# Optimization experiments

Measured on AMD Instinct MI355X. Metric: run time of the kernel, lower is better.

Reference implementation:

```python
import jax, jax.numpy as jnp
import numpy as np
import math

N_HEAD = 16
N_KV = 4


def setup_inputs() -> dict:
    key = jax.random.key(0)
    ks = jax.random.split(key, 10)
    B, T, C = 4, 2048, 1024
    hd = C // N_HEAD
    kv_dim = N_KV * hd  # 256
    s = 0.02
    return {
        "x": jax.random.normal(ks[0], (B, T, C), jnp.float32),
        "Wq": jax.random.normal(ks[1], (C, C), jnp.float32) * s,
        "bq": jax.random.normal(ks[2], (C,), jnp.float32) * s,
        "Wk": jax.random.normal(ks[3], (kv_dim, C), jnp.float32) * s,
        "bk": jax.random.normal(ks[4], (kv_dim,), jnp.float32) * s,
        "Wv": jax.random.normal(ks[5], (kv_dim, C), jnp.float32) * s,
        "bv": jax.random.normal(ks[6], (kv_dim,), jnp.float32) * s,
        "Wo": jax.random.normal(ks[7], (C, C), jnp.float32) * s,
        "bo": jax.random.normal(ks[8], (C,), jnp.float32) * s,
        "qk_gain": jnp.full((N_HEAD,), 5.5, jnp.float32),
    }


def reference(x, Wq, bq, Wk, bk, Wv, bv, Wo, bo, qk_gain):
    B, T, C = x.shape
    H, KV = N_HEAD, N_KV
    hd = C // H
    G = H // KV  # GQA group size

    # Projections (torch Linear: y = x @ W.T + b)
    q = (x @ Wq.T + bq).reshape(B, T, KV, G, hd).transpose(0, 2, 3, 1, 4)  # [B,KV,G,T,hd]
    k = (x @ Wk.T + bk).reshape(B, T, KV, hd).transpose(0, 2, 1, 3)        # [B,KV,T,hd]
    v = (x @ Wv.T + bv).reshape(B, T, KV, hd).transpose(0, 2, 1, 3)        # [B,KV,T,hd]

    # per-head gain on q; head order h = kv*G + g matches repeat_interleave
    q = q * qk_gain.reshape(1, KV, G, 1, 1)

    # GQA: contract each query group against its shared kv head (no KV replication)
    att = jnp.einsum('bkgtd,bksd->bkgts', q, k) / math.sqrt(hd)  # [B,KV,G,T,T]
    causal = jnp.tril(jnp.ones((T, T), bool))
    att = jnp.where(causal, att, -jnp.inf)
    att = jax.nn.softmax(att, axis=-1)

    y = jnp.einsum('bkgts,bksd->bkgtd', att, v)          # [B,KV,G,T,hd]
    y = y.transpose(0, 3, 1, 2, 4).reshape(B, T, C)      # [B,T,C]
    return y @ Wo.T + bo
```

## Files before the change

kernel.cpp:

```cpp
#include <hip/hip_runtime.h>
#include <hip/hip_bf16.h>

typedef __attribute__((ext_vector_type(8))) short bf16x8;
typedef __attribute__((ext_vector_type(4))) float f32x4;
typedef __attribute__((ext_vector_type(16))) float f32x16;
typedef __attribute__((ext_vector_type(2))) unsigned uint2v;

#define DEVI static __device__ __forceinline__

constexpr int Bb = 4, Tt = 2048, Cc = 1024, Hh = 16;
constexpr int Mrows = Bb * Tt;
constexpr int KVdim = 256;
constexpr float LOG2E = 1.44269504088896340736f;

DEVI unsigned short f2bf(float f) {
  union { float f; unsigned u; } v; v.f = f;
  unsigned r = v.u + 0x7fffu + ((v.u >> 16) & 1u);
  return (unsigned short)(r >> 16);
}

DEVI f32x4 mfma16(bf16x8 a, bf16x8 b, f32x4 c) {
  return __builtin_amdgcn_mfma_f32_16x16x32_bf16(a, b, c, 0, 0, 0);
}
DEVI f32x16 mfma32(bf16x8 a, bf16x8 b, f32x16 c) {
  return __builtin_amdgcn_mfma_f32_32x32x16_bf16(a, b, c, 0, 0, 0);
}

DEVI unsigned cvtpk(float lo, float hi) {
  unsigned w;
  asm("v_cvt_pk_bf16_f32 %0, %1, %2" : "=v"(w) : "v"(lo), "v"(hi));
  return w;
}

DEVI void load_lds16(const void* g, void* s) {
  __builtin_amdgcn_global_load_lds(
      (const __attribute__((address_space(1))) void*)g,
      (__attribute__((address_space(3))) void*)s, 16, 0, 0);
}

__global__ __launch_bounds__(256) void cvt_all(
    const float* __restrict__ s0, const float* __restrict__ s1,
    const float* __restrict__ s2, const float* __restrict__ s3,
    const float* __restrict__ s4,
    unsigned short* __restrict__ d0, unsigned short* __restrict__ d1,
    unsigned short* __restrict__ d2, unsigned short* __restrict__ d3,
    unsigned short* __restrict__ d4,
    int n0, int n1, int n2, int n3, int n4) {
  const float* s; unsigned short* d; int n;
  switch (blockIdx.y) {
    case 0: s = s0; d = d0; n = n0; break;
    case 1: s = s1; d = d1; n = n1; break;
    case 2: s = s2; d = d2; n = n2; break;
    case 3: s = s3; d = d3; n = n3; break;
    default: s = s4; d = d4; n = n4; break;
  }
  int i = (blockIdx.x * 256 + threadIdx.x) * 4;
  const int stride = gridDim.x * 256 * 4;
  for (; i < n; i += stride) {
    float4 v = *(const float4*)(s + i);
    ushort4 o;
    o.x = f2bf(v.x); o.y = f2bf(v.y); o.z = f2bf(v.z); o.w = f2bf(v.w);
    *(ushort4*)(d + i) = o;
  }
}

__global__ __launch_bounds__(256, 4) void qkv_gemm(const short* __restrict__ A,
                                                const short* __restrict__ wq,
                                                const short* __restrict__ wk,
                                                const short* __restrict__ wv,
                                                const float* __restrict__ bq,
                                                const float* __restrict__ bk,
                                                const float* __restrict__ bv,
                                                const float* __restrict__ gain,
                                                unsigned short* __restrict__ qout,
                                                unsigned short* __restrict__ kout,
                                                unsigned short* __restrict__ vout) {
  constexpr int K = Cc;
  __shared__ __align__(16) union QkvSmem {
    struct { short As[128 * 64]; short Bs[128 * 64]; } g;
    unsigned short Ls[64][136];
  } sm;
  short* As = sm.g.As;
  short* Bs = sm.g.Bs;
  const int tid = threadIdx.x;
  const int w = tid >> 6, l = tid & 63;
  const int l15 = l & 15, lg = l >> 4;
  const int m0 = blockIdx.x * 128, n0 = blockIdx.y * 128;

  const short* Bsrc; const float* bias; int mode;
  if (n0 < 1024)      { Bsrc = wq + (size_t)n0 * K;          bias = bq + n0;          mode = 0; }
  else if (n0 < 1280) { Bsrc = wk + (size_t)(n0 - 1024) * K; bias = bk + (n0 - 1024); mode = 1; }
  else                { Bsrc = wv + (size_t)(n0 - 1280) * K; bias = bv + (n0 - 1280); mode = 2; }

  const int wr = (w >> 1) * 64, wc = (w & 1) * 64;
  f32x4 acc[4][4] = {};

  const int lrow = l >> 3;
  const int lchk = (l & 7) ^ (lrow & 7);
  const short* gA = A + (size_t)(m0 + w * 32 + lrow) * K + lchk * 8;
  const short* gB = Bsrc + (size_t)(w * 32 + lrow) * K + lchk * 8;
  short* lA = As + w * 32 * 64;
  short* lB = Bs + w * 32 * 64;
  const int sw = l15 & 7;

  for (int k0 = 0; k0 < K; k0 += 64) {
#pragma unroll
    for (int i = 0; i < 4; ++i) {
      load_lds16(gA + (size_t)i * 8 * K, lA + i * 8 * 64);
      load_lds16(gB + (size_t)i * 8 * K, lB + i * 8 * 64);
    }
    gA += 64; gB += 64;
    __syncthreads();
    bf16x8 af[2][4], bfr[2][4];
#pragma unroll
    for (int kk = 0; kk < 2; ++kk)
#pragma unroll
      for (int i = 0; i < 4; ++i) {
        const int ch = ((kk * 4 + lg) ^ sw) << 3;
        af[kk][i] = *(const bf16x8*)(As + (wr + i * 16 + l15) * 64 + ch);
        bfr[kk][i] = *(const bf16x8*)(Bs + (wc + i * 16 + l15) * 64 + ch);
      }
#pragma unroll
    for (int kk = 0; kk < 2; ++kk)
#pragma unroll
      for (int mi = 0; mi < 4; ++mi)
#pragma unroll
        for (int ni = 0; ni < 4; ++ni)
          acc[mi][ni] = mfma16(af[kk][mi], bfr[kk][ni], acc[mi][ni]);
    __syncthreads();
  }

  const int crow = m0 + wr + lg * 4;
  if (mode == 2) {
    const int bb2 = m0 >> 11, tt0 = m0 & (Tt - 1);
#pragma unroll
    for (int colHalf = 0; colHalf < 2; ++colHalf) {
      if (colHalf) __syncthreads();
      if ((w & 1) == colHalf) {
#pragma unroll
        for (int ni = 0; ni < 4; ++ni) {
          const int c = ni * 16 + l15;
          const float bv_ = bias[colHalf * 64 + c];
#pragma unroll
          for (int mi = 0; mi < 4; ++mi)
#pragma unroll
            for (int r = 0; r < 4; ++r)
              sm.Ls[c][wr + lg * 4 + mi * 16 + r] = f2bf(acc[mi][ni][r] + bv_);
        }
      }
      __syncthreads();
      const int c = tid >> 2, ch = tid & 3;
      const int vcol = (n0 - 1280) + colHalf * 64 + c;
      unsigned short* dst = vout +
          ((size_t)((bb2 * 4 + (vcol >> 6)) * 64 + (vcol & 63))) * Tt + tt0 + ch * 32;
      const unsigned short* src = &sm.Ls[c][ch * 32];
#pragma unroll
      for (int q = 0; q < 4; ++q)
        *(bf16x8*)(dst + q * 8) = *(const bf16x8*)(src + q * 8);
    }
    return;
  }
#pragma unroll
  for (int ni = 0; ni < 4; ++ni) {
    const int lcol = wc + ni * 16 + l15;
    const float bv_ = bias[lcol];
    float sc = 1.f;
    if (mode == 0) sc = gain[(n0 + lcol) >> 6] * 0.125f * LOG2E;
#pragma unroll
    for (int mi = 0; mi < 4; ++mi) {
#pragma unroll
      for (int r = 0; r < 4; ++r) {
        const int row = crow + mi * 16 + r;
        float v = acc[mi][ni][r] + bv_;
        if (mode == 0) {
          qout[(size_t)row * Cc + n0 + lcol] = f2bf(v * sc);
        } else {
          kout[(size_t)row * KVdim + (n0 - 1024) + lcol] = f2bf(v);
        }
      }
    }
  }
}

__global__ __launch_bounds__(256, 4) void gemm_o(const short* __restrict__ A,
                                              const short* __restrict__ Bw,
                                              const float* __restrict__ bias,
                                              float* __restrict__ Cout,
                                              int M, int N, int K) {
  __shared__ __align__(16) short As[128 * 64];
  __shared__ __align__(16) short Bs[128 * 64];
  const int tid = threadIdx.x;
  const int w = tid >> 6, l = tid & 63;
  const int l15 = l & 15, lg = l >> 4;
  const int m0 = blockIdx.x * 128, n0 = blockIdx.y * 128;
  const int wr = (w >> 1) * 64, wc = (w & 1) * 64;
  f32x4 acc[4][4] = {};

  const int lrow = l >> 3;
  const int lchk = (l & 7) ^ (lrow & 7);
  const short* gA = A + (size_t)(m0 + w * 32 + lrow) * K + lchk * 8;
  const short* gB = Bw + (size_t)(n0 + w * 32 + lrow) * K + lchk * 8;
  short* lA = As + w * 32 * 64;
  short* lB = Bs + w * 32 * 64;
  const int sw = l15 & 7;

  for (int k0 = 0; k0 < K; k0 += 64) {
#pragma unroll
    for (int i = 0; i < 4; ++i) {
      load_lds16(gA + (size_t)i * 8 * K, lA + i * 8 * 64);
      load_lds16(gB + (size_t)i * 8 * K, lB + i * 8 * 64);
    }
    gA += 64; gB += 64;
    __syncthreads();
    bf16x8 af[2][4], bfr[2][4];
#pragma unroll
    for (int kk = 0; kk < 2; ++kk)
#pragma unroll
      for (int i = 0; i < 4; ++i) {
        const int ch = ((kk * 4 + lg) ^ sw) << 3;
        af[kk][i] = *(const bf16x8*)(As + (wr + i * 16 + l15) * 64 + ch);
        bfr[kk][i] = *(const bf16x8*)(Bs + (wc + i * 16 + l15) * 64 + ch);
      }
#pragma unroll
    for (int kk = 0; kk < 2; ++kk)
#pragma unroll
      for (int mi = 0; mi < 4; ++mi)
#pragma unroll
        for (int ni = 0; ni < 4; ++ni)
          acc[mi][ni] = mfma16(af[kk][mi], bfr[kk][ni], acc[mi][ni]);
    __syncthreads();
  }

  const int crow = m0 + wr + lg * 4;
  const int ccol = n0 + wc + l15;
#pragma unroll
  for (int ni = 0; ni < 4; ++ni) {
    const int col = ccol + ni * 16;
    const float bv = bias[col];
#pragma unroll
    for (int mi = 0; mi < 4; ++mi)
#pragma unroll
      for (int r = 0; r < 4; ++r)
        Cout[(size_t)(crow + mi * 16 + r) * N + col] = acc[mi][ni][r] + bv;
  }
}

#define PACK_SUB(pp, dst)                                        \
  {                                                              \
    unsigned Aw = cvtpk(pp[0], pp[1]), Bw_ = cvtpk(pp[2], pp[3]);\
    unsigned Cw = cvtpk(pp[4], pp[5]), Dw = cvtpk(pp[6], pp[7]); \
    uint2v xc = __builtin_amdgcn_permlane32_swap(Aw, Cw, false, false); \
    uint2v yd = __builtin_amdgcn_permlane32_swap(Bw_, Dw, false, false);\
    dst[0] = xc[0]; dst[1] = yd[0]; dst[2] = xc[1]; dst[3] = yd[1];     \
    Aw = cvtpk(pp[8], pp[9]); Bw_ = cvtpk(pp[10], pp[11]);       \
    Cw = cvtpk(pp[12], pp[13]); Dw = cvtpk(pp[14], pp[15]);      \
    xc = __builtin_amdgcn_permlane32_swap(Aw, Cw, false, false); \
    yd = __builtin_amdgcn_permlane32_swap(Bw_, Dw, false, false);\
    dst[4] = xc[0]; dst[5] = yd[0]; dst[6] = xc[1]; dst[7] = yd[1];     \
  }

#define HALF(ROFF, CB)                                                        \
  {                                                                           \
    f32x16 sa = {};                                                           \
    _Pragma("unroll")                                                         \
    for (int c = 0; c < 4; ++c) {                                             \
      bf16x8 ka = *(const bf16x8*)&Ks[kpar][(ROFF) + l31][c * 16 + hi * 8];   \
      sa = mfma32(ka, qf[c], sa);                                             \
    }                                                                         \
    if (s0 + (ROFF) + 31 > qw0) {                                             \
      _Pragma("unroll")                                                       \
      for (int r = 0; r < 16; ++r) {                                          \
        const int sl = s0 + (ROFF) + (r & 3) + 8 * (r >> 2) + 4 * hi;         \
        if (sl > q_abs) sa[r] = -1e30f;                                       \
      }                                                                       \
    }                                                                         \
    _Pragma("unroll")                                                         \
    for (int r = 0; r < 16; ++r) sa[r] = exp2f(sa[r]);                        \
    {                                                                         \
      float a0 = (sa[0] + sa[1]) + (sa[2] + sa[3]);                           \
      float a1 = (sa[4] + sa[5]) + (sa[6] + sa[7]);                           \
      float a2 = (sa[8] + sa[9]) + (sa[10] + sa[11]);                         \
      float a3 = (sa[12] + sa[13]) + (sa[14] + sa[15]);                       \
      l_s += (a0 + a1) + (a2 + a3);                                           \
    }                                                                         \
    unsigned pw[8];                                                           \
    PACK_SUB(sa, pw);                                                         \
    _Pragma("unroll")                                                         \
    for (int t4 = 0; t4 < 2; ++t4) {                                          \
      union { unsigned u[4]; bf16x8 v; } pb;                                  \
      pb.u[0] = pw[t4 * 4 + 0]; pb.u[1] = pw[t4 * 4 + 1];                     \
      pb.u[2] = pw[t4 * 4 + 2]; pb.u[3] = pw[t4 * 4 + 3];                     \
      bf16x8 va0 = *(const bf16x8*)&Vt[kpar][l31][((CB) + t4) * 16 + hi * 8]; \
      bf16x8 va1 = *(const bf16x8*)&Vt[kpar][32 + l31][((CB) + t4) * 16 + hi * 8];\
      ot0 = mfma32(va0, pb.v, ot0);                                           \
      ot1 = mfma32(va1, pb.v, ot1);                                           \
    }                                                                         \
  }

__global__ __launch_bounds__(512, 4) void attn9(const short* __restrict__ qb,
                                                const short* __restrict__ kb,
                                                const short* __restrict__ vtg,
                                                unsigned short* __restrict__ ob) {
  __shared__ __align__(16) union SmemU {
    struct { short Ks[2][64][72]; short Vt[2][64][72]; } s;
    struct { float red[256 * 32]; float redl[256]; } r;
  } sm;
  auto& Ks = sm.s.Ks;
  auto& Vt = sm.s.Vt;

  const int tid = threadIdx.x, w = tid >> 6, l = tid & 63;
  const int l31 = l & 31, hi = l >> 5;
  const int qsub = w & 3, kpar = w >> 2;
  const int id = blockIdx.x;
  const int bh = id & 63, j = id >> 6;
  const int perm[16] = {15, 14, 13, 12, 8, 9, 10, 11, 7, 6, 5, 4, 0, 1, 2, 3};
  const int i128 = perm[j];
  const int b = bh >> 4, h = bh & 15, kv = h >> 2;
  const int q0 = i128 * 128;
  const int qw0 = q0 + qsub * 32;
  const int q_abs = qw0 + l31;

  const short* qp = qb + (size_t)(b * Tt + q_abs) * Cc + h * 64 + hi * 8;
  bf16x8 qf[4];
#pragma unroll
  for (int c = 0; c < 4; ++c) qf[c] = *(const bf16x8*)(qp + c * 16);

  f32x16 ot0 = {}, ot1 = {};
  float l_s = 0.f;

  const int half512 = tid >> 8;
  const int srow = (tid & 255) >> 2, scol = (tid & 3) * 16;
  const short* kst = kb + (size_t)(b * Tt + srow) * KVdim + kv * 64 + scol;
  const short* vst = vtg + (size_t)((b * 4 + kv) * 64 + srow) * Tt + scol;

  const int ntiles = 2 * i128 + 2;

  bf16x8 rk0, rk1, rv0, rv1;
  {
    const short* ks = kst + (size_t)half512 * 64 * KVdim;
    const short* vs = vst + half512 * 64;
    rk0 = *(const bf16x8*)ks;  rk1 = *(const bf16x8*)(ks + 8);
    rv0 = *(const bf16x8*)vs;  rv1 = *(const bf16x8*)(vs + 8);
  }

  for (int tp = 0; tp < ntiles; tp += 2) {
    *(bf16x8*)&Ks[half512][srow][scol] = rk0;
    *(bf16x8*)&Ks[half512][srow][scol + 8] = rk1;
    *(bf16x8*)&Vt[half512][srow][scol] = rv0;
    *(bf16x8*)&Vt[half512][srow][scol + 8] = rv1;
    __syncthreads();
    const int ts = tp + 2 + half512;
    if (ts < ntiles) {
      const short* ks = kst + (size_t)ts * 64 * KVdim;
      const short* vs = vst + ts * 64;
      rk0 = *(const bf16x8*)ks;  rk1 = *(const bf16x8*)(ks + 8);
      rv0 = *(const bf16x8*)vs;  rv1 = *(const bf16x8*)(vs + 8);
    }
    const int t = tp + kpar;
    if (t < ntiles) {
      const int s0 = t * 64;
      if (s0 <= qw0 + 31) {
        HALF(0, 0);
        if (s0 + 32 <= qw0 + 31) HALF(32, 2);
      }
    }
    __syncthreads();
  }

  float* red = sm.r.red;
  float* redl = sm.r.redl;
  const int rot = l & 7;
  if (kpar == 1) {
    float* p = red + ((qsub * 64 + l) * 32);
#pragma unroll
    for (int c = 0; c < 8; ++c) {
      const int cc = ((c + rot) & 7) * 4;
      f32x4 v;
      if (c < 4) {
        v[0] = ot0[c * 4]; v[1] = ot0[c * 4 + 1];
        v[2] = ot0[c * 4 + 2]; v[3] = ot0[c * 4 + 3];
      } else {
        const int b0 = (c - 4) * 4;
        v[0] = ot1[b0]; v[1] = ot1[b0 + 1];
        v[2] = ot1[b0 + 2]; v[3] = ot1[b0 + 3];
      }
      *(f32x4*)(p + cc) = v;
    }
    redl[qsub * 64 + l] = l_s;
  }
  __syncthreads();
  if (kpar == 0) {
    const float* p = red + ((qsub * 64 + l) * 32);
#pragma unroll
    for (int c = 0; c < 8; ++c) {
      const int cc = ((c + rot) & 7) * 4;
      f32x4 v = *(const f32x4*)(p + cc);
      if (c < 4) {
        ot0[c * 4] += v[0]; ot0[c * 4 + 1] += v[1];
        ot0[c * 4 + 2] += v[2]; ot0[c * 4 + 3] += v[3];
      } else {
        const int b0 = (c - 4) * 4;
        ot1[b0] += v[0]; ot1[b0 + 1] += v[1];
        ot1[b0 + 2] += v[2]; ot1[b0 + 3] += v[3];
      }
    }
    l_s += redl[qsub * 64 + l];
    l_s += __shfl_xor(l_s, 32);
    const float inv = 1.f / l_s;
    unsigned short* op = ob + (size_t)(b * Tt + q_abs) * Cc + h * 64;
#pragma unroll
    for (int r = 0; r < 16; ++r) {
      const int d = (r & 3) + 8 * (r >> 2) + 4 * hi;
      op[d] = f2bf(ot0[r] * inv);
      op[32 + d] = f2bf(ot1[r] * inv);
    }
  }
}

extern "C" void kernel_launch(void* const* d_in, const int* in_sizes, int n_in,
                              void* d_out, int out_size, void* d_ws, size_t ws_size,
                              hipStream_t stream) {
  (void)in_sizes; (void)n_in; (void)out_size; (void)ws_size;
  const float* x  = (const float*)d_in[0];
  const float* Wq = (const float*)d_in[1];
  const float* bq = (const float*)d_in[2];
  const float* Wk = (const float*)d_in[3];
  const float* bk = (const float*)d_in[4];
  const float* Wv = (const float*)d_in[5];
  const float* bv = (const float*)d_in[6];
  const float* Wo = (const float*)d_in[7];
  const float* bo = (const float*)d_in[8];
  const float* gain = (const float*)d_in[9];
  float* out = (float*)d_out;

  char* ws = (char*)d_ws;
  short* xb  = (short*)ws;                    ws += (size_t)Mrows * Cc * 2;
  short* qbf = (short*)ws;                    ws += (size_t)Mrows * Cc * 2;
  short* kbf = (short*)ws;                    ws += (size_t)Mrows * KVdim * 2;
  short* vtg = (short*)ws;                    ws += (size_t)Mrows * KVdim * 2;
  short* atb = (short*)ws;                    ws += (size_t)Mrows * Cc * 2;
  short* wqb = (short*)ws;                    ws += (size_t)Cc * Cc * 2;
  short* wkb = (short*)ws;                    ws += (size_t)KVdim * Cc * 2;
  short* wvb = (short*)ws;                    ws += (size_t)KVdim * Cc * 2;
  short* wob = (short*)ws;                    ws += (size_t)Cc * Cc * 2;

  cvt_all<<<dim3(1024, 5), 256, 0, stream>>>(
      x, Wq, Wk, Wv, Wo,
      (unsigned short*)xb, (unsigned short*)wqb, (unsigned short*)wkb,
      (unsigned short*)wvb, (unsigned short*)wob,
      Mrows * Cc, Cc * Cc, KVdim * Cc, KVdim * Cc, Cc * Cc);

  qkv_gemm<<<dim3(Mrows / 128, 12), 256, 0, stream>>>(
      xb, wqb, wkb, wvb, bq, bk, bv, gain,
      (unsigned short*)qbf, (unsigned short*)kbf, (unsigned short*)vtg);

  attn9<<<1024, 512, 0, stream>>>(qbf, kbf, vtg, (unsigned short*)atb);

  gemm_o<<<dim3(Mrows / 128, Cc / 128), 256, 0, stream>>>(
      atb, wob, bo, out, Mrows, Cc, Cc);
}
```

Baseline: 130.6 us.

## Quad-buffer attention K/V tiles in LDS and split GEMM fragment loads

The attention kernel moves from a 2-slot LDS ring to a 4-slot ring. Each tile pair is written to LDS one iteration ahead, and the next global load is issued two iterations ahead, so global loads and LDS writes are spread across loop iterations and overlap with compute. The point is to hide K/V fetch latency behind the QK/PV MFMA work. In exchange, shared memory per block roughly doubles, which may cut how many 512-thread blocks fit on a CU despite the launch bound. Both GEMM kernels also load the fragments for each k-half just before that half's MFMAs, which should lower register pressure.

```diff
diff --git a/kernel.cpp b/kernel.cpp
--- a/kernel.cpp
+++ b/kernel.cpp
@@ -111,22 +111,21 @@
     }
     gA += 64; gB += 64;
     __syncthreads();
-    bf16x8 af[2][4], bfr[2][4];
-#pragma unroll
-    for (int kk = 0; kk < 2; ++kk)
+#pragma unroll
+    for (int kk = 0; kk < 2; ++kk) {
+      bf16x8 af[4], bfr[4];
+      const int ch = ((kk * 4 + lg) ^ sw) << 3;
 #pragma unroll
       for (int i = 0; i < 4; ++i) {
-        const int ch = ((kk * 4 + lg) ^ sw) << 3;
-        af[kk][i] = *(const bf16x8*)(As + (wr + i * 16 + l15) * 64 + ch);
-        bfr[kk][i] = *(const bf16x8*)(Bs + (wc + i * 16 + l15) * 64 + ch);
-      }
-#pragma unroll
-    for (int kk = 0; kk < 2; ++kk)
+        af[i] = *(const bf16x8*)(As + (wr + i * 16 + l15) * 64 + ch);
+        bfr[i] = *(const bf16x8*)(Bs + (wc + i * 16 + l15) * 64 + ch);
+      }
 #pragma unroll
       for (int mi = 0; mi < 4; ++mi)
 #pragma unroll
         for (int ni = 0; ni < 4; ++ni)
-          acc[mi][ni] = mfma16(af[kk][mi], bfr[kk][ni], acc[mi][ni]);
+          acc[mi][ni] = mfma16(af[mi], bfr[ni], acc[mi][ni]);
+    }
     __syncthreads();
   }
 
@@ -212,22 +211,21 @@
     }
     gA += 64; gB += 64;
     __syncthreads();
-    bf16x8 af[2][4], bfr[2][4];
-#pragma unroll
-    for (int kk = 0; kk < 2; ++kk)
+#pragma unroll
+    for (int kk = 0; kk < 2; ++kk) {
+      bf16x8 af[4], bfr[4];
+      const int ch = ((kk * 4 + lg) ^ sw) << 3;
 #pragma unroll
       for (int i = 0; i < 4; ++i) {
-        const int ch = ((kk * 4 + lg) ^ sw) << 3;
-        af[kk][i] = *(const bf16x8*)(As + (wr + i * 16 + l15) * 64 + ch);
-        bfr[kk][i] = *(const bf16x8*)(Bs + (wc + i * 16 + l15) * 64 + ch);
-      }
-#pragma unroll
-    for (int kk = 0; kk < 2; ++kk)
+        af[i] = *(const bf16x8*)(As + (wr + i * 16 + l15) * 64 + ch);
+        bfr[i] = *(const bf16x8*)(Bs + (wc + i * 16 + l15) * 64 + ch);
+      }
 #pragma unroll
       for (int mi = 0; mi < 4; ++mi)
 #pragma unroll
         for (int ni = 0; ni < 4; ++ni)
-          acc[mi][ni] = mfma16(af[kk][mi], bfr[kk][ni], acc[mi][ni]);
+          acc[mi][ni] = mfma16(af[mi], bfr[ni], acc[mi][ni]);
+    }
     __syncthreads();
   }
 
@@ -259,12 +257,12 @@
     dst[4] = xc[0]; dst[5] = yd[0]; dst[6] = xc[1]; dst[7] = yd[1];     \
   }
 
-#define HALF(ROFF, CB)                                                        \
+#define HALF(BUF, ROFF, CB)                                                   \
   {                                                                           \
     f32x16 sa = {};                                                           \
     _Pragma("unroll")                                                         \
     for (int c = 0; c < 4; ++c) {                                             \
-      bf16x8 ka = *(const bf16x8*)&Ks[kpar][(ROFF) + l31][c * 16 + hi * 8];   \
+      bf16x8 ka = *(const bf16x8*)&Ks[BUF][(ROFF) + l31][c * 16 + hi * 8];    \
       sa = mfma32(ka, qf[c], sa);                                             \
     }                                                                         \
     if (s0 + (ROFF) + 31 > qw0) {                                             \
@@ -290,19 +288,19 @@
       union { unsigned u[4]; bf16x8 v; } pb;                                  \
       pb.u[0] = pw[t4 * 4 + 0]; pb.u[1] = pw[t4 * 4 + 1];                     \
       pb.u[2] = pw[t4 * 4 + 2]; pb.u[3] = pw[t4 * 4 + 3];                     \
-      bf16x8 va0 = *(const bf16x8*)&Vt[kpar][l31][((CB) + t4) * 16 + hi * 8]; \
-      bf16x8 va1 = *(const bf16x8*)&Vt[kpar][32 + l31][((CB) + t4) * 16 + hi * 8];\
+      bf16x8 va0 = *(const bf16x8*)&Vt[BUF][l31][((CB) + t4) * 16 + hi * 8];  \
+      bf16x8 va1 = *(const bf16x8*)&Vt[BUF][32 + l31][((CB) + t4) * 16 + hi * 8];\
       ot0 = mfma32(va0, pb.v, ot0);                                           \
       ot1 = mfma32(va1, pb.v, ot1);                                           \
     }                                                                         \
   }
 
-__global__ __launch_bounds__(512, 4) void attn9(const short* __restrict__ qb,
-                                                const short* __restrict__ kb,
-                                                const short* __restrict__ vtg,
-                                                unsigned short* __restrict__ ob) {
+__global__ __launch_bounds__(512, 4) void attn10(const short* __restrict__ qb,
+                                                 const short* __restrict__ kb,
+                                                 const short* __restrict__ vtg,
+                                                 unsigned short* __restrict__ ob) {
   __shared__ __align__(16) union SmemU {
-    struct { short Ks[2][64][72]; short Vt[2][64][72]; } s;
+    struct { short Ks[4][64][72]; short Vt[4][64][72]; } s;
     struct { float red[256 * 32]; float redl[256]; } r;
   } sm;
   auto& Ks = sm.s.Ks;
@@ -333,38 +331,42 @@
   const short* kst = kb + (size_t)(b * Tt + srow) * KVdim + kv * 64 + scol;
   const short* vst = vtg + (size_t)((b * 4 + kv) * 64 + srow) * Tt + scol;
 
-  const int ntiles = 2 * i128 + 2;
+  const int np = i128 + 1;
 
   bf16x8 rk0, rk1, rv0, rv1;
-  {
-    const short* ks = kst + (size_t)half512 * 64 * KVdim;
-    const short* vs = vst + half512 * 64;
-    rk0 = *(const bf16x8*)ks;  rk1 = *(const bf16x8*)(ks + 8);
-    rv0 = *(const bf16x8*)vs;  rv1 = *(const bf16x8*)(vs + 8);
-  }
-
-  for (int tp = 0; tp < ntiles; tp += 2) {
-    *(bf16x8*)&Ks[half512][srow][scol] = rk0;
-    *(bf16x8*)&Ks[half512][srow][scol + 8] = rk1;
-    *(bf16x8*)&Vt[half512][srow][scol] = rv0;
-    *(bf16x8*)&Vt[half512][srow][scol + 8] = rv1;
+#define LOADP(p)                                                   \
+  {                                                                \
+    const int ts_ = 2 * (p) + half512;                             \
+    const short* ks_ = kst + (size_t)ts_ * 64 * KVdim;             \
+    const short* vs_ = vst + ts_ * 64;                             \
+    rk0 = *(const bf16x8*)ks_;  rk1 = *(const bf16x8*)(ks_ + 8);   \
+    rv0 = *(const bf16x8*)vs_;  rv1 = *(const bf16x8*)(vs_ + 8);   \
+  }
+#define WRITEP(p)                                                  \
+  {                                                                \
+    const int bu_ = (2 * (p) + half512) & 3;                       \
+    *(bf16x8*)&Ks[bu_][srow][scol] = rk0;                          \
+    *(bf16x8*)&Ks[bu_][srow][scol + 8] = rk1;                      \
+    *(bf16x8*)&Vt[bu_][srow][scol] = rv0;                          \
+    *(bf16x8*)&Vt[bu_][srow][scol + 8] = rv1;                      \
+  }
+
+  LOADP(0); WRITEP(0);
+  if (np > 1) { LOADP(1); WRITEP(1); }
+  if (np > 2) LOADP(2);
+  __syncthreads();
+
+  for (int p = 0; p < np; ++p) {
+    const int t = 2 * p + kpar;
+    const int s0 = t * 64;
+    const int bu = t & 3;
+    if (s0 <= qw0 + 31) {
+      HALF(bu, 0, 0);
+      if (s0 + 32 <= qw0 + 31) HALF(bu, 32, 2);
+    }
     __syncthreads();
-    const int ts = tp + 2 + half512;
-    if (ts < ntiles) {
-      const short* ks = kst + (size_t)ts * 64 * KVdim;
-      const short* vs = vst + ts * 64;
-      rk0 = *(const bf16x8*)ks;  rk1 = *(const bf16x8*)(ks + 8);
-      rv0 = *(const bf16x8*)vs;  rv1 = *(const bf16x8*)(vs + 8);
-    }
-    const int t = tp + kpar;
-    if (t < ntiles) {
-      const int s0 = t * 64;
-      if (s0 <= qw0 + 31) {
-        HALF(0, 0);
-        if (s0 + 32 <= qw0 + 31) HALF(32, 2);
-      }
-    }
-    __syncthreads();
+    if (p + 2 < np) WRITEP(p + 2);
+    if (p + 3 < np) LOADP(p + 3);
   }
 
   float* red = sm.r.red;
@@ -454,7 +456,7 @@
       xb, wqb, wkb, wvb, bq, bk, bv, gain,
       (unsigned short*)qbf, (unsigned short*)kbf, (unsigned short*)vtg);
 
-  attn9<<<1024, 512, 0, stream>>>(qbf, kbf, vtg, (unsigned short*)atb);
+  attn10<<<1024, 512, 0, stream>>>(qbf, kbf, vtg, (unsigned short*)atb);
 
   gemm_o<<<dim3(Mrows / 128, Cc / 128), 256, 0, stream>>>(
       atb, wob, bo, out, Mrows, Cc, Cc);
```

Result: slower. 134.5 us (+3.0%).
